# Kernel optimization log

Measured on AMD Instinct MI355X. Metric: run time of the kernel, lower is better.

Reference implementation:

```python
import jax, jax.numpy as jnp
import numpy as np

N_NODES = 250_000
N_EDGES = 1_250_000
N_CRY = 50_000
EMB = 200
FEA = 64
HID = 256
N_GRAPH = 3
ELEM_HEADS = 3
CRY_HEADS = 3


def _simple_net(x, w1, b1, w2, b2):
    # SimpleNetwork([d_in, 256, d_out]): Linear -> LeakyReLU -> Linear
    h = jax.nn.leaky_relu(x @ w1 + b1, negative_slope=0.01)
    return h @ w2 + b2


def setup_inputs() -> dict:
    key = jax.random.key(0)
    ks = jax.random.split(key, 32)
    s = 0.05
    inp = {
        # weights strictly positive (fractional stoichiometry weights)
        "elem_weights": jax.random.uniform(ks[0], (N_NODES, 1), jnp.float32) * 0.9 + 0.05,
        "elem_fea": jax.random.normal(ks[1], (N_NODES, EMB), jnp.float32),
        "self_fea_idx": jax.random.randint(ks[2], (N_EDGES,), 0, N_NODES),
        "nbr_fea_idx": jax.random.randint(ks[3], (N_EDGES,), 0, N_NODES),
        "cry_elem_idx": jnp.sort(jax.random.randint(ks[4], (N_NODES,), 0, N_CRY)),
        # embedding: Linear(EMB, FEA-1)
        "emb_w": jax.random.normal(ks[5], (EMB, FEA - 1), jnp.float32) * s,
        "emb_b": jnp.zeros((FEA - 1,), jnp.float32),
        # graph-layer attention heads (n_graph, elem_heads, ...)
        "g_gate_w1": jax.random.normal(ks[6], (N_GRAPH, ELEM_HEADS, 2 * FEA, HID), jnp.float32) * s,
        "g_gate_b1": jnp.zeros((N_GRAPH, ELEM_HEADS, HID), jnp.float32),
        "g_gate_w2": jax.random.normal(ks[7], (N_GRAPH, ELEM_HEADS, HID, 1), jnp.float32) * s,
        "g_gate_b2": jnp.zeros((N_GRAPH, ELEM_HEADS, 1), jnp.float32),
        "g_msg_w1": jax.random.normal(ks[8], (N_GRAPH, ELEM_HEADS, 2 * FEA, HID), jnp.float32) * s,
        "g_msg_b1": jnp.zeros((N_GRAPH, ELEM_HEADS, HID), jnp.float32),
        "g_msg_w2": jax.random.normal(ks[9], (N_GRAPH, ELEM_HEADS, HID, FEA), jnp.float32) * s,
        "g_msg_b2": jnp.zeros((N_GRAPH, ELEM_HEADS, FEA), jnp.float32),
        "g_pow": jax.random.normal(ks[10], (N_GRAPH, ELEM_HEADS), jnp.float32),
        # crystal pooling heads
        "c_gate_w1": jax.random.normal(ks[11], (CRY_HEADS, FEA, HID), jnp.float32) * s,
        "c_gate_b1": jnp.zeros((CRY_HEADS, HID), jnp.float32),
        "c_gate_w2": jax.random.normal(ks[12], (CRY_HEADS, HID, 1), jnp.float32) * s,
        "c_gate_b2": jnp.zeros((CRY_HEADS, 1), jnp.float32),
        "c_msg_w1": jax.random.normal(ks[13], (CRY_HEADS, FEA, HID), jnp.float32) * s,
        "c_msg_b1": jnp.zeros((CRY_HEADS, HID), jnp.float32),
        "c_msg_w2": jax.random.normal(ks[14], (CRY_HEADS, HID, FEA), jnp.float32) * s,
        "c_msg_b2": jnp.zeros((CRY_HEADS, FEA), jnp.float32),
        "c_pow": jax.random.normal(ks[15], (CRY_HEADS,), jnp.float32),
    }
    return inp


def _attn_pool(fea, weights, index, num_segments, gw1, gb1, gw2, gb2, mw1, mb1, mw2, mb2, p):
    # WeightedAttentionPooling: scatter-softmax with (weights ** pow) factor
    gate = _simple_net(fea, gw1, gb1, gw2, gb2)                       # (E, 1)
    gmax = jax.ops.segment_max(gate, index, num_segments=num_segments)
    gate = (weights ** p) * jnp.exp(gate - gmax[index])
    den = jax.ops.segment_sum(gate, index, num_segments=num_segments)
    gate = gate / (den[index] + 1e-10)
    msg = _simple_net(fea, mw1, mb1, mw2, mb2)                        # (E, FEA)
    return jax.ops.segment_sum(gate * msg, index, num_segments=num_segments)


def reference(elem_weights, elem_fea, self_fea_idx, nbr_fea_idx, cry_elem_idx,
              emb_w, emb_b,
              g_gate_w1, g_gate_b1, g_gate_w2, g_gate_b2,
              g_msg_w1, g_msg_b1, g_msg_w2, g_msg_b2, g_pow,
              c_gate_w1, c_gate_b1, c_gate_w2, c_gate_b2,
              c_msg_w1, c_msg_b1, c_msg_w2, c_msg_b2, c_pow):
    n = elem_fea.shape[0]
    x = elem_fea @ emb_w + emb_b                                      # (N, FEA-1)
    x = jnp.concatenate([x, elem_weights], axis=1)                    # (N, FEA)
    w_nbr = elem_weights[nbr_fea_idx]                                 # (M, 1)
    for l in range(g_pow.shape[0]):
        fea = jnp.concatenate([x[self_fea_idx], x[nbr_fea_idx]], axis=1)  # (M, 2*FEA)
        heads = []
        for h in range(g_pow.shape[1]):
            heads.append(_attn_pool(
                fea, w_nbr, self_fea_idx, n,
                g_gate_w1[l, h], g_gate_b1[l, h], g_gate_w2[l, h], g_gate_b2[l, h],
                g_msg_w1[l, h], g_msg_b1[l, h], g_msg_w2[l, h], g_msg_b2[l, h],
                g_pow[l, h]))
        x = jnp.mean(jnp.stack(heads), axis=0) + x                    # residual
    heads = []
    for h in range(c_pow.shape[0]):
        heads.append(_attn_pool(
            x, elem_weights, cry_elem_idx, N_CRY,
            c_gate_w1[h], c_gate_b1[h], c_gate_w2[h], c_gate_b2[h],
            c_msg_w1[h], c_msg_b1[h], c_msg_w2[h], c_msg_b2[h],
            c_pow[h]))
    return jnp.mean(jnp.stack(heads), axis=0)                         # (C, FEA)
```

## Files before the change

### kernel.cpp

```cpp
#include <hip/hip_runtime.h>
#include <math.h>

#define NN 250000
#define NE 1250000
#define NC 50000
#define EMBD 200
#define NCH 245
#define NBLK 22000
#define SSTR ((size_t)NBLK * 64)

typedef unsigned int u32;
typedef unsigned short u16;
typedef short s16x8 __attribute__((ext_vector_type(8)));
typedef float f32x4 __attribute__((ext_vector_type(4)));

__device__ __forceinline__ u16 f2bf(float f) {
    u32 u = __float_as_uint(f);
    return (u16)((u + 0x7FFFu + ((u >> 16) & 1u)) >> 16);
}
__device__ __forceinline__ float bf2f(u16 u) { return __uint_as_float(((u32)u) << 16); }
__device__ __forceinline__ u32 cvtpk(float lo, float hi) {
    u32 r;
    asm("v_cvt_pk_bf16_f32 %0, %1, %2" : "=v"(r) : "v"(lo), "v"(hi));
    return r;
}
__device__ __forceinline__ float lrelu(float v) { return v > 0.f ? v : 0.01f * v; }
__device__ __forceinline__ u32 encf(float f) {
    u32 u = __float_as_uint(f);
    return (u & 0x80000000u) ? ~u : (u | 0x80000000u);
}
__device__ __forceinline__ float decf(u32 k) {
    return __uint_as_float((k & 0x80000000u) ? (k ^ 0x80000000u) : ~k);
}

__global__ void k_pack(const float* __restrict__ src, u16* __restrict__ dst,
                       int K, int N, int nheads)
{
    const int t = blockIdx.x * 256 + threadIdx.x;
    const int F = (K / 32) * (N / 16);
    if (t >= nheads * F * 64) return;
    const int lane = t & 63;
    const int fh = t >> 6;
    const int f = fh % F, head = fh / F;
    const int ng = f % (N / 16), ks = f / (N / 16);
    const int q = lane >> 4, c = lane & 15;
    const float* s = src + (size_t)head * K * N;
    u16 o[8];
    #pragma unroll
    for (int i = 0; i < 8; ++i)
        o[i] = f2bf(s[(size_t)(32 * ks + 8 * q + i) * N + 16 * ng + c]);
    uint4 v;
    v.x = (u32)o[0] | ((u32)o[1] << 16);
    v.y = (u32)o[2] | ((u32)o[3] << 16);
    v.z = (u32)o[4] | ((u32)o[5] << 16);
    v.w = (u32)o[6] | ((u32)o[7] << 16);
    *(uint4*)(dst + (size_t)head * K * N + ((size_t)f * 64 + lane) * 8) = v;
// ... 119 lines not shown
            const int row = m * 16 + c;
            const int g = (ks * 4 + q) ^ (row & 7);
            s16x8 ah = *(const s16x8*)((const char*)Ahi + row * 512 + g * 16);
            s16x8 al = *(const s16x8*)((const char*)Alo + row * 512 + g * 16);
            acc[m] = __builtin_amdgcn_mfma_f32_16x16x32_bf16(ah, B[ks], acc[m], 0, 0, 0);
            acc[m] = __builtin_amdgcn_mfma_f32_16x16x32_bf16(al, B[ks], acc[m], 0, 0, 0);
        }
    }
    const int col = w * 16 + c;
    const float bv = (col < 63) ? emb_b[col] : 0.f;
    #pragma unroll
    for (int m = 0; m < 4; ++m)
        #pragma unroll
        for (int r = 0; r < 4; ++r) {
            const int node = n0 + m * 16 + q * 4 + r;
            if (node < NN) {
                const float val = (col < 63) ? acc[m][r] + bv : elem_w[node];
                x[(size_t)node * 64 + col] = val;
                xbf[(size_t)node * 64 + col] = f2bf(val);
            }
        }
}

__global__ void k_deg(const int* __restrict__ self_idx, int* __restrict__ deg) {
    int e = blockIdx.x * 256 + threadIdx.x;
    if (e < NE) atomicAdd(&deg[self_idx[e]], 1);
}

__global__ void k_nodepack(const int* __restrict__ deg, int* __restrict__ nstart,
                           int* __restrict__ ctotal)
{
    __shared__ int sdeg[1024];
    __shared__ int sst[1024];
    const int c0 = blockIdx.x << 10;
    const int cnt = min(1024, NN - c0);
    for (int i = threadIdx.x; i < cnt; i += 64) sdeg[i] = deg[c0 + i];
    __syncthreads();
    if (threadIdx.x == 0) {
        int cur = 0;
        for (int i = 0; i < cnt; ++i) {
            int d = sdeg[i];
            if (d > 0 && ((cur & 63) + d > 64)) cur = (cur + 63) & ~63;
            sst[i] = cur;
            cur += d;
        }
        ctotal[blockIdx.x] = (cur + 63) & ~63;
    }
    __syncthreads();
    for (int i = threadIdx.x; i < cnt; i += 64) nstart[c0 + i] = sst[i];
}

__global__ void k_chunkscan(const int* __restrict__ ctotal, int* __restrict__ cbase) {
    __shared__ int s[256];
    int t = threadIdx.x;
    int v = (t < NCH) ? ctotal[t] : 0;
    s[t] = v;
    __syncthreads();
    for (int off = 1; off < 256; off <<= 1) {
        int add = (t >= off) ? s[t - off] : 0;
        __syncthreads();
        s[t] += add;
        __syncthreads();
    }
    if (t < NCH) cbase[t] = s[t] - v;
}

__global__ void k_fill(const int* __restrict__ self_idx, const int* __restrict__ nbr_idx,
                       const float* __restrict__ elem_w,
                       const int* __restrict__ nstart, const int* __restrict__ cbase,
                       int* __restrict__ cursor, int2* __restrict__ gnode,
                       float* __restrict__ gwn)
{
    int e = blockIdx.x * 256 + threadIdx.x;
    if (e >= NE) return;
    int n = self_idx[e];
    int r = atomicAdd(&cursor[n], 1);
    int slot = cbase[n >> 10] + nstart[n] + r;
    int nb = nbr_idx[e];
    gnode[slot] = make_int2(n, nb);
    gwn[slot] = elem_w[nb];
}

__global__ __launch_bounds__(256, 4) void k_lgate(
    const u16* __restrict__ xbf, const int2* __restrict__ gnode,
    const float* __restrict__ gwn,
    const u16* __restrict__ gw1p, const float* __restrict__ gb1,
    const u16* __restrict__ gw2p, const float* __restrict__ gpw,
    float* __restrict__ sgf_out)
{
    __shared__ __align__(16) u16 sA[64 * 128];
    __shared__ __align__(16) u16 sH[64 * 128];
    __shared__ float sg[4][64];
    __shared__ float gfin[64], tval[64];
    __shared__ float swn[64];
    __shared__ int   snid[64];
    __shared__ short srs[64], sre[64];
    const int tid = threadIdx.x;
    const int base = blockIdx.x * 64;
    if (gnode[base].x < 0) return;

    if (tid < 64) {
        int2 nn = gnode[base + tid];
        snid[tid] = nn.x;
        swn[tid] = gwn[base + tid];
    }
    for (int i = tid; i < 64 * 16; i += 256) {
        const int row = i >> 4, g = i & 15;
        const int2 nn = gnode[base + row];
        const int node = (g < 8) ? nn.x : nn.y;
        uint4 v; v.x = 0; v.y = 0; v.z = 0; v.w = 0;
        if (node >= 0) v = *(const uint4*)(xbf + (size_t)node * 64 + (g & 7) * 8);
        *(uint4*)((char*)sA + row * 256 + ((g ^ (row & 7)) * 16)) = v;
    }
    __syncthreads();
    if (tid < 64) {
        int n = snid[tid];
        int rs = tid, re = tid + 1;
        if (n >= 0) {
            while (rs > 0 && snid[rs - 1] == n) --rs;
            while (re < 64 && snid[re] == n) ++re;
        }
        srs[tid] = (short)rs; sre[tid] = (short)re;
    }

    const int w = tid >> 6, lane = tid & 63, q = lane >> 4, c = lane & 15;

    #pragma unroll 1
    for (int h = 0; h < 3; ++h) {
        f32x4 acc2[4];
        #pragma unroll
        for (int m = 0; m < 4; ++m) acc2[m] = 0.f;
        const u16* wp = gw1p + (size_t)h * 128 * 256;
        #pragma unroll 1
        for (int half = 0; half < 2; ++half) {
            f32x4 acc[4][2];
            #pragma unroll
            for (int m = 0; m < 4; ++m) { acc[m][0] = 0.f; acc[m][1] = 0.f; }
            __builtin_amdgcn_s_setprio(1);
            #pragma unroll 2
            for (int ks = 0; ks < 4; ++ks) {
                s16x8 B1[2];
                #pragma unroll
                for (int n2 = 0; n2 < 2; ++n2)
                    B1[n2] = *(const s16x8*)(wp + ((size_t)(ks * 16 + w * 4 + half * 2 + n2) * 64 + lane) * 8);
                s16x8 a[4];
                #pragma unroll
                for (int m = 0; m < 4; ++m) {
                    const int row = m * 16 + c;
                    a[m] = *(const s16x8*)((const char*)sA + row * 256 + (((ks * 4 + q) ^ (row & 7)) * 16));
                }
                #pragma unroll
                for (int n2 = 0; n2 < 2; ++n2)
                    #pragma unroll
                    for (int m = 0; m < 4; ++m)
                        acc[m][n2] = __builtin_amdgcn_mfma_f32_16x16x32_bf16(a[m], B1[n2], acc[m][n2], 0, 0, 0);
            }
            __builtin_amdgcn_s_setprio(0);

            __syncthreads();
            const float b1a = gb1[h * 256 + w * 64 + (half * 2 + 0) * 16 + c];
            const float b1b = gb1[h * 256 + w * 64 + (half * 2 + 1) * 16 + c];
            #pragma unroll
            for (int m = 0; m < 4; ++m)
                #pragma unroll
                for (int r = 0; r < 4; ++r) {
                    const int row = m * 16 + q * 4 + r;
                    const u32 pk = cvtpk(lrelu(acc[m][0][r] + b1a), lrelu(acc[m][1][r] + b1b));
                    *(u32*)((char*)sH + row * 256 + (((w * 4 + (c >> 2)) ^ (row & 7)) * 16) + (c & 3) * 4) = pk;
                }
            s16x8 B2 = *(const s16x8*)(gw2p + ((size_t)(h * 8 + half * 4 + w) * 64 + lane) * 8);
            __syncthreads();

// ... 8 lines not shown
        }
        if (c == 0) {
            #pragma unroll
            for (int m = 0; m < 4; ++m)
                #pragma unroll
                for (int r = 0; r < 4; ++r)
                    sg[w][m * 16 + q * 4 + r] = acc2[m][r];
        }
        __syncthreads();
        if (tid < 64)
            gfin[tid] = (snid[tid] >= 0) ? sg[0][tid] + sg[1][tid] + sg[2][tid] + sg[3][tid] : -1e30f;
        __syncthreads();
        if (tid < 64) {
            const int rs = srs[tid], re = sre[tid];
            float m = -1e30f;
            for (int j = rs; j < re; ++j) m = fmaxf(m, gfin[j]);
            tval[tid] = (snid[tid] >= 0) ? powf(swn[tid], gpw[h]) * expf(gfin[tid] - m) : 0.f;
        }
        __syncthreads();
        if (tid < 64) {
            const int rs = srs[tid], re = sre[tid];
            float d = 1e-10f;
            for (int j = rs; j < re; ++j) d += tval[j];
            sgf_out[SSTR * h + base + tid] = tval[tid] / d;
        }
        __syncthreads();
    }
}

__global__ __launch_bounds__(256, 4) void k_lmsg(
    const u16* __restrict__ xbf, const int2* __restrict__ gnode,
    const u16* __restrict__ mw1p, const float* __restrict__ mb1,
    const u16* __restrict__ mw2p, const float* __restrict__ mb2,
    const float* __restrict__ sgf_in, float* __restrict__ pooled)
{
    __shared__ __align__(16) u16 sA[64 * 128];
    __shared__ __align__(16) u16 sH[64 * 128];
    __shared__ float sgfl[64][3];
    __shared__ int   snid[64];
    __shared__ short srs[64], sre[64];
    const int tid = threadIdx.x;
    const int base = blockIdx.x * 64;
    if (gnode[base].x < 0) return;

    if (tid < 64) snid[tid] = gnode[base + tid].x;
    if (tid < 192) {
        const int row = tid / 3, h = tid % 3;
        sgfl[row][h] = sgf_in[SSTR * h + base + row];
    }
    for (int i = tid; i < 64 * 16; i += 256) {
        const int row = i >> 4, g = i & 15;
        const int2 nn = gnode[base + row];
        const int node = (g < 8) ? nn.x : nn.y;
        uint4 v; v.x = 0; v.y = 0; v.z = 0; v.w = 0;
        if (node >= 0) v = *(const uint4*)(xbf + (size_t)node * 64 + (g & 7) * 8);
        *(uint4*)((char*)sA + row * 256 + ((g ^ (row & 7)) * 16)) = v;
    }
    __syncthreads();
    if (tid < 64) {
        int n = snid[tid];
        int rs = tid, re = tid + 1;
        if (n >= 0) {
            while (rs > 0 && snid[rs - 1] == n) --rs;
            while (re < 64 && snid[re] == n) ++re;
        }
        srs[tid] = (short)rs; sre[tid] = (short)re;
    }

    const int w = tid >> 6, lane = tid & 63, q = lane >> 4, c = lane & 15;
    float wacc[4][4];
    #pragma unroll
    for (int m = 0; m < 4; ++m)
        #pragma unroll
        for (int r = 0; r < 4; ++r) wacc[m][r] = 0.f;

    #pragma unroll 1
    for (int h = 0; h < 3; ++h) {
        const u16* wp = mw1p + (size_t)h * 128 * 256;
        #pragma unroll 1
        for (int half = 0; half < 2; ++half) {
            f32x4 acc[4][2];
            #pragma unroll
            for (int m = 0; m < 4; ++m) { acc[m][0] = 0.f; acc[m][1] = 0.f; }
            __builtin_amdgcn_s_setprio(1);
            #pragma unroll 2
            for (int ks = 0; ks < 4; ++ks) {
                s16x8 B1[2];
                #pragma unroll
                for (int n2 = 0; n2 < 2; ++n2)
                    B1[n2] = *(const s16x8*)(wp + ((size_t)(ks * 16 + w * 4 + half * 2 + n2) * 64 + lane) * 8);
                s16x8 a[4];
                #pragma unroll
                for (int m = 0; m < 4; ++m) {
                    const int row = m * 16 + c;
                    a[m] = *(const s16x8*)((const char*)sA + row * 256 + (((ks * 4 + q) ^ (row & 7)) * 16));
                }
                #pragma unroll
                for (int n2 = 0; n2 < 2; ++n2)
                    #pragma unroll
                    for (int m = 0; m < 4; ++m)
                        acc[m][n2] = __builtin_amdgcn_mfma_f32_16x16x32_bf16(a[m], B1[n2], acc[m][n2], 0, 0, 0);
            }
            __builtin_amdgcn_s_setprio(0);

            __syncthreads();
            const float b1a = mb1[h * 256 + w * 64 + (half * 2 + 0) * 16 + c];
            const float b1b = mb1[h * 256 + w * 64 + (half * 2 + 1) * 16 + c];
            #pragma unroll
            for (int m = 0; m < 4; ++m)
                #pragma unroll
                for (int r = 0; r < 4; ++r) {
                    const int row = m * 16 + q * 4 + r;
                    const u32 pk = cvtpk(lrelu(acc[m][0][r] + b1a), lrelu(acc[m][1][r] + b1b));
                    *(u32*)((char*)sH + row * 256 + (((w * 4 + (c >> 2)) ^ (row & 7)) * 16) + (c & 3) * 4) = pk;
                }
            s16x8 B2[4];
            #pragma unroll
            for (int k2 = 0; k2 < 4; ++k2)
// ... 21 lines not shown
                for (int r = 0; r < 4; ++r) {
                    const int row = m2 * 16 + q * 4 + r;
                    wacc[m2][r] += (acc2[m2][r] + b2v) * sgfl[row][h];
                }
        }
        __syncthreads();
    }

    float* waccL = (float*)sH;
    #pragma unroll
    for (int m = 0; m < 4; ++m)
        #pragma unroll
        for (int r = 0; r < 4; ++r)
            waccL[(m * 16 + q * 4 + r) * 64 + w * 16 + c] = wacc[m][r];
    __syncthreads();
    {
        const int col = tid & 63, grp = tid >> 6;
        for (int i = grp; i < 64; i += 4) {
            const int n = snid[i];
            if (n >= 0 && srs[i] == (short)i) {
                float s = 0.f;
                const int re = sre[i];
                for (int j = i; j < re; ++j) s += waccL[j * 64 + col];
                pooled[(size_t)n * 64 + col] = s * (1.f / 3.f);
            }
        }
    }
}

__global__ void k_mirror2(float* __restrict__ x, const float* __restrict__ pooled,
                          u16* __restrict__ xbf, int n4)
{
    int i = blockIdx.x * 256 + threadIdx.x;
    if (i >= n4) return;
    float4 xv = *(const float4*)(x + (size_t)i * 4);
    float4 pv = *(const float4*)(pooled + (size_t)i * 4);
    xv.x += pv.x; xv.y += pv.y; xv.z += pv.z; xv.w += pv.w;
    *(float4*)(x + (size_t)i * 4) = xv;
    uint2 o;
    o.x = cvtpk(xv.x, xv.y);
    o.y = cvtpk(xv.z, xv.w);
    *(uint2*)(xbf + (size_t)i * 4) = o;
}

template<int KD, bool GATHER>
__global__ __launch_bounds__(256, 4) void k_gate(
    const u16* __restrict__ xbf, const int* __restrict__ sidx, const int* __restrict__ nidx,
    const int* __restrict__ scat, const u16* __restrict__ w1p,
    const float* __restrict__ b1g, const float* __restrict__ w2g,
    float* __restrict__ gate_out, u32* __restrict__ gmax, int nrows, size_t gstride)
{
    constexpr int KS = KD / 32;
    constexpr int RB = KD * 2;
    constexpr int G  = KD / 8;
    __shared__ __align__(16) u16 sA[64 * KD];
    __shared__ float sg[4][64];
    const int tid = threadIdx.x;
    const int r0 = blockIdx.x * 64;
    const int rem = min(64, nrows - r0);

    for (int i = tid; i < 64 * G; i += 256) {
        const int row = i / G, g = i % G;
        const int rr = (row < rem) ? row : 0;
        uint4 v;
        if (GATHER) {
            const int node = (g < G / 2) ? sidx[r0 + rr] : nidx[r0 + rr];
            v = *(const uint4*)(xbf + (size_t)node * 64 + (g & (G / 2 - 1)) * 8);
        } else {
            v = *(const uint4*)(xbf + (size_t)(r0 + rr) * 64 + g * 8);
        }
        *(uint4*)((char*)sA + row * RB + ((g ^ (row & 7)) * 16)) = v;
    }
    __syncthreads();

    const int w = tid >> 6, lane = tid & 63, q = lane >> 4, c = lane & 15;

    #pragma unroll 1
    for (int h = 0; h < 3; ++h) {
        float part[4][4];
        #pragma unroll
        for (int m = 0; m < 4; ++m)
            #pragma unroll
            for (int r = 0; r < 4; ++r) part[m][r] = 0.f;
        const u16* wp = w1p + (size_t)h * KD * 256;
        #pragma unroll 1
        for (int half = 0; half < 2; ++half) {
            f32x4 acc[4][2];
            #pragma unroll
            for (int m = 0; m < 4; ++m) { acc[m][0] = 0.f; acc[m][1] = 0.f; }
            __builtin_amdgcn_s_setprio(1);
            #pragma unroll 2
            for (int ks = 0; ks < KS; ++ks) {
                s16x8 B1[2];
                #pragma unroll
                for (int n2 = 0; n2 < 2; ++n2)
                    B1[n2] = *(const s16x8*)(wp + ((size_t)(ks * 16 + w * 4 + half * 2 + n2) * 64 + lane) * 8);
                s16x8 a[4];
                #pragma unroll
                for (int m = 0; m < 4; ++m) {
                    const int row = m * 16 + c;
                    a[m] = *(const s16x8*)((const char*)sA + row * RB + (((ks * 4 + q) ^ (row & 7)) * 16));
                }
                #pragma unroll
                for (int n2 = 0; n2 < 2; ++n2)
                    #pragma unroll
                    for (int m = 0; m < 4; ++m)
                        acc[m][n2] = __builtin_amdgcn_mfma_f32_16x16x32_bf16(a[m], B1[n2], acc[m][n2], 0, 0, 0);
            }
            __builtin_amdgcn_s_setprio(0);
            #pragma unroll
            for (int n2 = 0; n2 < 2; ++n2) {
                const int col = w * 64 + (half * 2 + n2) * 16 + c;
                const float b1v = b1g[h * 256 + col];
                const float w2v = w2g[h * 256 + col];
                #pragma unroll
                for (int m = 0; m < 4; ++m)
                    #pragma unroll
                    for (int r = 0; r < 4; ++r)
                        part[m][r] += lrelu(acc[m][n2][r] + b1v) * w2v;
            }
        }
        #pragma unroll
        for (int off = 1; off < 16; off <<= 1)
            #pragma unroll
            for (int m = 0; m < 4; ++m)
                #pragma unroll
                for (int r = 0; r < 4; ++r)
                    part[m][r] += __shfl_xor(part[m][r], off, 64);
        if (c == 0) {
            #pragma unroll
            for (int m = 0; m < 4; ++m)
                #pragma unroll
                for (int r = 0; r < 4; ++r)
                    sg[w][m * 16 + q * 4 + r] = part[m][r];
        }
        __syncthreads();
        if (tid < rem) {
            const float gv = sg[0][tid] + sg[1][tid] + sg[2][tid] + sg[3][tid];
            gate_out[gstride * h + r0 + tid] = gv;
            atomicMax(&gmax[scat[r0 + tid] * 3 + h], encf(gv));
        }
        __syncthreads();
    }
}

template<int KD, bool GATHER>
__global__ __launch_bounds__(256, 4) void k_msg(
    const u16* __restrict__ xbf, const int* __restrict__ sidx, const int* __restrict__ nidx,
    const int* __restrict__ scat, const u16* __restrict__ w1p, const float* __restrict__ b1g,
    const u16* __restrict__ w2p, const float* __restrict__ b2g,
    const float* __restrict__ tbuf, const float* __restrict__ den,
    float* __restrict__ outp, int nrows, size_t gstride)
{
    constexpr int KS = KD / 32;
    constexpr int RB = KD * 2;
    constexpr int G  = KD / 8;
    __shared__ __align__(16) u16 sA[64 * KD];
    __shared__ __align__(16) u16 sH[64 * 128];
    __shared__ float sgf[64][3];
    __shared__ int ssi[64];
    const int tid = threadIdx.x;
    const int r0 = blockIdx.x * 64;
    const int rem = min(64, nrows - r0);

    for (int i = tid; i < 64 * G; i += 256) {
        const int row = i / G, g = i % G;
        const int rr = (row < rem) ? row : 0;
        uint4 v;
        if (GATHER) {
            const int node = (g < G / 2) ? sidx[r0 + rr] : nidx[r0 + rr];
            v = *(const uint4*)(xbf + (size_t)node * 64 + (g & (G / 2 - 1)) * 8);
        } else {
            v = *(const uint4*)(xbf + (size_t)(r0 + rr) * 64 + g * 8);
        }
        *(uint4*)((char*)sA + row * RB + ((g ^ (row & 7)) * 16)) = v;
    }
    if (tid < 64) ssi[tid] = (tid < rem) ? scat[r0 + tid] : 0;
    if (tid < 192) {
        const int row = tid / 3, h = tid % 3;
        if (row < rem) {
            const int s = scat[r0 + row] * 3 + h;
            sgf[row][h] = tbuf[gstride * h + r0 + row] / (den[s] + 1e-10f);
        } else {
            sgf[row][h] = 0.f;
        }
    }
    __syncthreads();

    const int w = tid >> 6, lane = tid & 63, q = lane >> 4, c = lane & 15;
    float wacc[4][4];
    #pragma unroll
    for (int m = 0; m < 4; ++m)
        #pragma unroll
        for (int r = 0; r < 4; ++r) wacc[m][r] = 0.f;

    #pragma unroll 1
    for (int h = 0; h < 3; ++h) {
        const u16* wp = w1p + (size_t)h * KD * 256;
        #pragma unroll 1
        for (int half = 0; half < 2; ++half) {
            f32x4 acc[4][2];
            #pragma unroll
            for (int m = 0; m < 4; ++m) { acc[m][0] = 0.f; acc[m][1] = 0.f; }
            __builtin_amdgcn_s_setprio(1);
            #pragma unroll 2
            for (int ks = 0; ks < KS; ++ks) {
                s16x8 B1[2];
                #pragma unroll
                for (int n2 = 0; n2 < 2; ++n2)
                    B1[n2] = *(const s16x8*)(wp + ((size_t)(ks * 16 + w * 4 + half * 2 + n2) * 64 + lane) * 8);
                s16x8 a[4];
                #pragma unroll
                for (int m = 0; m < 4; ++m) {
                    const int row = m * 16 + c;
                    a[m] = *(const s16x8*)((const char*)sA + row * RB + (((ks * 4 + q) ^ (row & 7)) * 16));
                }
                #pragma unroll
                for (int n2 = 0; n2 < 2; ++n2)
                    #pragma unroll
                    for (int m = 0; m < 4; ++m)
                        acc[m][n2] = __builtin_amdgcn_mfma_f32_16x16x32_bf16(a[m], B1[n2], acc[m][n2], 0, 0, 0);
            }
            __builtin_amdgcn_s_setprio(0);

            __syncthreads();
            const float b1a = b1g[h * 256 + w * 64 + (half * 2 + 0) * 16 + c];
            const float b1b = b1g[h * 256 + w * 64 + (half * 2 + 1) * 16 + c];
            #pragma unroll
            for (int m = 0; m < 4; ++m)
                #pragma unroll
                for (int r = 0; r < 4; ++r) {
                    const int row = m * 16 + q * 4 + r;
                    const u32 pk = cvtpk(lrelu(acc[m][0][r] + b1a), lrelu(acc[m][1][r] + b1b));
                    *(u32*)((char*)sH + row * 256 + (((w * 4 + (c >> 2)) ^ (row & 7)) * 16) + (c & 3) * 4) = pk;
                }
            s16x8 B2[4];
            #pragma unroll
            for (int k2 = 0; k2 < 4; ++k2)
                B2[k2] = *(const s16x8*)(w2p + (size_t)h * 256 * 64 + ((size_t)((half * 4 + k2) * 4 + w) * 64 + lane) * 8);
            __syncthreads();

            f32x4 acc2[4];
            #pragma unroll
            for (int m = 0; m < 4; ++m) acc2[m] = 0.f;
            __builtin_amdgcn_s_setprio(1);
            #pragma unroll
            for (int k2 = 0; k2 < 4; ++k2) {
                #pragma unroll
                for (int m2 = 0; m2 < 4; ++m2) {
                    const int row = m2 * 16 + c;
                    s16x8 a2 = *(const s16x8*)((const char*)sH + row * 256 + (((k2 * 4 + q) ^ (row & 7)) * 16));
                    acc2[m2] = __builtin_amdgcn_mfma_f32_16x16x32_bf16(a2, B2[k2], acc2[m2], 0, 0, 0);
                }
            }
            __builtin_amdgcn_s_setprio(0);
            const float b2v = half ? b2g[h * 64 + w * 16 + c] : 0.f;
            #pragma unroll
            for (int m2 = 0; m2 < 4; ++m2)
                #pragma unroll
                for (int r = 0; r < 4; ++r) {
                    const int row = m2 * 16 + q * 4 + r;
                    wacc[m2][r] += (acc2[m2][r] + b2v) * sgf[row][h];
                }
        }
    }
    #pragma unroll
    for (int m = 0; m < 4; ++m)
        #pragma unroll
        for (int r = 0; r < 4; ++r) {
            const int row = m * 16 + q * 4 + r;
            if (row < rem)
                atomicAdd(&outp[(size_t)ssi[row] * 64 + w * 16 + c], wacc[m][r] * (1.f / 3.f));
        }
}

__global__ void k_seg_exp(float* __restrict__ gate_t, const int* __restrict__ idx,
                          const int* __restrict__ wi, const float* __restrict__ elem_w,
                          const float* __restrict__ pw, const u32* __restrict__ gmax,
                          float* __restrict__ den, int n, size_t gstride)
{
    int e = blockIdx.x * blockDim.x + threadIdx.x;
    if (e >= n) return;
    int s = idx[e] * 3;
    float wgt = elem_w[wi ? wi[e] : e];
    #pragma unroll
    for (int h = 0; h < 3; ++h) {
        float gm = decf(gmax[s + h]);
        float t = powf(wgt, pw[h]) * expf(gate_t[gstride * h + e] - gm);
        gate_t[gstride * h + e] = t;
        atomicAdd(&den[s + h], t);
    }
}

extern "C" void kernel_launch(void* const* d_in, const int* in_sizes, int n_in,
                              void* d_out, int out_size, void* d_ws, size_t ws_size,
                              hipStream_t stream)
{
    const float* elem_w   = (const float*)d_in[0];
    const float* elem_fea = (const float*)d_in[1];
    const int*   self_idx = (const int*)d_in[2];
    const int*   nbr_idx  = (const int*)d_in[3];
    const int*   cry_idx  = (const int*)d_in[4];
    const float* emb_w    = (const float*)d_in[5];
    const float* emb_b    = (const float*)d_in[6];
    const float* gg_w1    = (const float*)d_in[7];
    const float* gg_b1    = (const float*)d_in[8];
    const float* gg_w2    = (const float*)d_in[9];
    const float* gm_w1    = (const float*)d_in[11];
    const float* gm_b1    = (const float*)d_in[12];
    const float* gm_w2    = (const float*)d_in[13];
    const float* gm_b2    = (const float*)d_in[14];
    const float* g_pow    = (const float*)d_in[15];
    const float* cg_w1    = (const float*)d_in[16];
    const float* cg_b1    = (const float*)d_in[17];
    const float* cg_w2    = (const float*)d_in[18];
    const float* cm_w1    = (const float*)d_in[20];
    const float* cm_b1    = (const float*)d_in[21];
    const float* cm_w2    = (const float*)d_in[22];
    const float* cm_b2    = (const float*)d_in[23];
    const float* c_pow    = (const float*)d_in[24];

    char* wsp = (char*)d_ws;
    size_t off = 0;
    auto alloc = [&](size_t b) { char* p = wsp + off; off += (b + 255) & ~(size_t)255; return p; };
    float* x      = (float*)alloc((size_t)NN * 64 * 4);
    float* pooled = (float*)alloc((size_t)NN * 64 * 4);
    u16*   xbf    = (u16*)  alloc((size_t)NN * 64 * 2);
    float* sgf    = (float*)alloc((size_t)3 * SSTR * 4);
    float* gate_t = (float*)alloc((size_t)NN * 3 * 4);
    float* cden   = (float*)alloc((size_t)NC * 3 * 4);
    u32*   cgmax  = (u32*)  alloc((size_t)NC * 3 * 4);
    int* deg    = (int*)alloc((size_t)NN * 4);
    int* nstart = (int*)alloc((size_t)NN * 4);
    int* cursor = (int*)alloc((size_t)NN * 4);
    int* ctotal = (int*)alloc((size_t)NCH * 4);
    int* cbase  = (int*)alloc((size_t)NCH * 4);
    int2* gnode = (int2*)alloc((size_t)NBLK * 64 * 8);
    float* gwn  = (float*)alloc((size_t)NBLK * 64 * 4);
    u16* wg1p = (u16*)alloc((size_t)9 * 128 * 256 * 2);
    u16* wm1p = (u16*)alloc((size_t)9 * 128 * 256 * 2);
    u16* wm2p = (u16*)alloc((size_t)9 * 256 * 64 * 2);
    u16* wg2p = (u16*)alloc((size_t)9 * 8 * 64 * 8 * 2);
    u16* cg1p = (u16*)alloc((size_t)3 * 64 * 256 * 2);
    u16* cm1p = (u16*)alloc((size_t)3 * 64 * 256 * 2);
    u16* cm2p = (u16*)alloc((size_t)3 * 256 * 64 * 2);
    u16* webp = (u16*)alloc((size_t)224 * 64 * 2);

    auto pack = [&](const float* s, u16* d, int K, int N, int H) {
        int tot = H * (K / 32) * (N / 16) * 64;
        k_pack<<<(tot + 255) / 256, 256, 0, stream>>>(s, d, K, N, H);
    };
    pack(gg_w1, wg1p, 128, 256, 9);
    pack(gm_w1, wm1p, 128, 256, 9);
    pack(cg_w1, cg1p, 64, 256, 3);
    pack(cm_w1, cm1p, 64, 256, 3);
    k_pack2<<<(9 * 32 * 64 + 255) / 256, 256, 0, stream>>>(gm_w2, wm2p, 9);
    k_pack2<<<(3 * 32 * 64 + 255) / 256, 256, 0, stream>>>(cm_w2, cm2p, 3);
    k_packg<<<(9 * 8 * 64 + 255) / 256, 256, 0, stream>>>(gg_w2, wg2p, 9);
    k_packe<<<7, 256, 0, stream>>>(emb_w, webp);

    hipMemsetAsync(deg, 0, (size_t)NN * 4, stream);
    hipMemsetAsync(cursor, 0, (size_t)NN * 4, stream);
    hipMemsetAsync(gnode, 0xFF, (size_t)NBLK * 64 * 8, stream);
    k_deg<<<(NE + 255) / 256, 256, 0, stream>>>(self_idx, deg);
    k_nodepack<<<NCH, 64, 0, stream>>>(deg, nstart, ctotal);
    k_chunkscan<<<1, 256, 0, stream>>>(ctotal, cbase);
    k_fill<<<(NE + 255) / 256, 256, 0, stream>>>(self_idx, nbr_idx, elem_w,
                                                 nstart, cbase, cursor, gnode, gwn);

    k_embed_mm<<<(NN + 63) / 64, 256, 0, stream>>>(elem_fea, elem_w, webp, emb_b, x, xbf);

    for (int l = 0; l < 3; ++l) {
        hipMemsetAsync(pooled, 0, (size_t)NN * 64 * 4, stream);
        k_lgate<<<NBLK, 256, 0, stream>>>(
            xbf, gnode, gwn,
            wg1p + (size_t)l * 3 * 128 * 256, gg_b1 + l * 768,
            wg2p + (size_t)l * 3 * 8 * 64 * 8, g_pow + l * 3, sgf);
        k_lmsg<<<NBLK, 256, 0, stream>>>(
            xbf, gnode,
            wm1p + (size_t)l * 3 * 128 * 256, gm_b1 + l * 768,
            wm2p + (size_t)l * 3 * 256 * 64, gm_b2 + l * 192, sgf, pooled);
        k_mirror2<<<(NN * 64 / 4 + 255) / 256, 256, 0, stream>>>(x, pooled, xbf, NN * 64 / 4);
    }

    hipMemsetAsync(cgmax, 0, (size_t)NC * 3 * 4, stream);
    hipMemsetAsync(cden, 0, (size_t)NC * 3 * 4, stream);
    hipMemsetAsync(d_out, 0, (size_t)NC * 64 * 4, stream);
    const int GN = (NN + 63) / 64;
    k_gate<64, false><<<GN, 256, 0, stream>>>(
        xbf, nullptr, nullptr, cry_idx, cg1p, cg_b1, cg_w2, gate_t, cgmax, NN, (size_t)NN);
    k_seg_exp<<<(NN + 255) / 256, 256, 0, stream>>>(
        gate_t, cry_idx, nullptr, elem_w, c_pow, cgmax, cden, NN, (size_t)NN);
    k_msg<64, false><<<GN, 256, 0, stream>>>(
        xbf, nullptr, nullptr, cry_idx, cm1p, cm_b1, cm2p, cm_b2,
        gate_t, cden, (float*)d_out, NN, (size_t)NN);
}
```

Before: 3.988 ms.

## Reuse segment-packed gate/msg kernels for crystal pooling and fuse residual add

Builds a segment-packed layout (blocks of 64 rows aligned to crystal boundaries) for the crystal pooling stage, so the templated in-block softmax gate and message kernels replace the old atomicMax/seg_exp/atomicAdd three-kernel path. The layer message kernel now adds directly into x, which removes the pooled buffer, its memset and the residual add in the mirror kernel. This costs extra setup kernels and some padding rows, and the crystal path now needs every crystal segment to fit within 64 rows.

```diff
diff --git a/kernel.cpp b/kernel.cpp
--- a/kernel.cpp
+++ b/kernel.cpp
@@ -5,9 +5,12 @@
 #define NE 1250000
 #define NC 50000
 #define EMBD 200
-#define NCH 245
+#define NCH_E 245
+#define NCH_C 49
 #define NBLK 22000
-#define SSTR ((size_t)NBLK * 64)
+#define NCBLK 6000
+#define SSTR  ((size_t)NBLK * 64)
+#define SSTRC ((size_t)NCBLK * 64)
 
 typedef unsigned int u32;
 typedef unsigned short u16;
@@ -25,13 +28,6 @@
     return r;
 }
 __device__ __forceinline__ float lrelu(float v) { return v > 0.f ? v : 0.01f * v; }
-__device__ __forceinline__ u32 encf(float f) {
-    u32 u = __float_as_uint(f);
-    return (u & 0x80000000u) ? ~u : (u | 0x80000000u);
-}
-__device__ __forceinline__ float decf(u32 k) {
-    return __uint_as_float((k & 0x80000000u) ? (k ^ 0x80000000u) : ~k);
-}
 
 __global__ void k_pack(const float* __restrict__ src, u16* __restrict__ dst,
                        int K, int N, int nheads)
@@ -197,18 +193,18 @@
         }
 }
 
-__global__ void k_deg(const int* __restrict__ self_idx, int* __restrict__ deg) {
+__global__ void k_deg(const int* __restrict__ idx, int* __restrict__ deg, int n) {
     int e = blockIdx.x * 256 + threadIdx.x;
-    if (e < NE) atomicAdd(&deg[self_idx[e]], 1);
+    if (e < n) atomicAdd(&deg[idx[e]], 1);
 }
 
 __global__ void k_nodepack(const int* __restrict__ deg, int* __restrict__ nstart,
-                           int* __restrict__ ctotal)
+                           int* __restrict__ ctotal, int total_n)
 {
     __shared__ int sdeg[1024];
     __shared__ int sst[1024];
     const int c0 = blockIdx.x << 10;
-    const int cnt = min(1024, NN - c0);
+    const int cnt = min(1024, total_n - c0);
     for (int i = threadIdx.x; i < cnt; i += 64) sdeg[i] = deg[c0 + i];
     __syncthreads();
     if (threadIdx.x == 0) {
@@ -225,10 +221,10 @@
     for (int i = threadIdx.x; i < cnt; i += 64) nstart[c0 + i] = sst[i];
 }
 
-__global__ void k_chunkscan(const int* __restrict__ ctotal, int* __restrict__ cbase) {
+__global__ void k_chunkscan(const int* __restrict__ ctotal, int* __restrict__ cbase, int nch) {
     __shared__ int s[256];
     int t = threadIdx.x;
-    int v = (t < NCH) ? ctotal[t] : 0;
+    int v = (t < nch) ? ctotal[t] : 0;
     s[t] = v;
     __syncthreads();
     for (int off = 1; off < 256; off <<= 1) {
@@ -237,7 +233,7 @@
         s[t] += add;
         __syncthreads();
     }
-    if (t < NCH) cbase[t] = s[t] - v;
+    if (t < nch) cbase[t] = s[t] - v;
 }
 
 __global__ void k_fill(const int* __restrict__ self_idx, const int* __restrict__ nbr_idx,
@@ -256,14 +252,32 @@
     gwn[slot] = elem_w[nb];
 }
 
+__global__ void k_cfill(const int* __restrict__ cry_idx, const float* __restrict__ elem_w,
+                        const int* __restrict__ nstart, const int* __restrict__ cbase,
+                        int* __restrict__ cursor, int2* __restrict__ gnode,
+                        float* __restrict__ gwn)
+{
+    int n = blockIdx.x * 256 + threadIdx.x;
+    if (n >= NN) return;
+    int cg = cry_idx[n];
+    int r = atomicAdd(&cursor[cg], 1);
+    int slot = cbase[cg >> 10] + nstart[cg] + r;
+    gnode[slot] = make_int2(cg, n);
+    gwn[slot] = elem_w[n];
+}
+
+template<int KD>
 __global__ __launch_bounds__(256, 4) void k_lgate(
     const u16* __restrict__ xbf, const int2* __restrict__ gnode,
     const float* __restrict__ gwn,
     const u16* __restrict__ gw1p, const float* __restrict__ gb1,
     const u16* __restrict__ gw2p, const float* __restrict__ gpw,
-    float* __restrict__ sgf_out)
-{
-    __shared__ __align__(16) u16 sA[64 * 128];
+    float* __restrict__ sgf_out, size_t sstr)
+{
+    constexpr int KS = KD / 32;
+    constexpr int G  = KD / 8;
+    constexpr int RB = KD * 2;
+    __shared__ __align__(16) u16 sA[64 * KD];
     __shared__ __align__(16) u16 sH[64 * 128];
     __shared__ float sg[4][64];
     __shared__ float gfin[64], tval[64];
@@ -279,13 +293,13 @@
         snid[tid] = nn.x;
         swn[tid] = gwn[base + tid];
     }
-    for (int i = tid; i < 64 * 16; i += 256) {
-        const int row = i >> 4, g = i & 15;
+    for (int i = tid; i < 64 * G; i += 256) {
+        const int row = i / G, g = i % G;
         const int2 nn = gnode[base + row];
-        const int node = (g < 8) ? nn.x : nn.y;
+        const int node = (KD == 128) ? ((g < 8) ? nn.x : nn.y) : nn.y;
         uint4 v; v.x = 0; v.y = 0; v.z = 0; v.w = 0;
         if (node >= 0) v = *(const uint4*)(xbf + (size_t)node * 64 + (g & 7) * 8);
-        *(uint4*)((char*)sA + row * 256 + ((g ^ (row & 7)) * 16)) = v;
+        *(uint4*)((char*)sA + row * RB + ((g ^ (row & 7)) * 16)) = v;
     }
     __syncthreads();
     if (tid < 64) {
@@ -305,7 +319,7 @@
         f32x4 acc2[4];
         #pragma unroll
         for (int m = 0; m < 4; ++m) acc2[m] = 0.f;
-        const u16* wp = gw1p + (size_t)h * 128 * 256;
+        const u16* wp = gw1p + (size_t)h * KD * 256;
         #pragma unroll 1
         for (int half = 0; half < 2; ++half) {
             f32x4 acc[4][2];
@@ -313,7 +327,7 @@
             for (int m = 0; m < 4; ++m) { acc[m][0] = 0.f; acc[m][1] = 0.f; }
             __builtin_amdgcn_s_setprio(1);
             #pragma unroll 2
-            for (int ks = 0; ks < 4; ++ks) {
+            for (int ks = 0; ks < KS; ++ks) {
                 s16x8 B1[2];
                 #pragma unroll
                 for (int n2 = 0; n2 < 2; ++n2)
@@ -322,7 +336,7 @@
                 #pragma unroll
                 for (int m = 0; m < 4; ++m) {
                     const int row = m * 16 + c;
-                    a[m] = *(const s16x8*)((const char*)sA + row * 256 + (((ks * 4 + q) ^ (row & 7)) * 16));
+                    a[m] = *(const s16x8*)((const char*)sA + row * RB + (((ks * 4 + q) ^ (row & 7)) * 16));
                 }
                 #pragma unroll
                 for (int n2 = 0; n2 < 2; ++n2)
@@ -377,19 +391,23 @@
             const int rs = srs[tid], re = sre[tid];
             float d = 1e-10f;
             for (int j = rs; j < re; ++j) d += tval[j];
-            sgf_out[SSTR * h + base + tid] = tval[tid] / d;
+            sgf_out[sstr * h + base + tid] = tval[tid] / d;
         }
         __syncthreads();
     }
 }
 
+template<int KD, bool RESID>
 __global__ __launch_bounds__(256, 4) void k_lmsg(
     const u16* __restrict__ xbf, const int2* __restrict__ gnode,
     const u16* __restrict__ mw1p, const float* __restrict__ mb1,
     const u16* __restrict__ mw2p, const float* __restrict__ mb2,
-    const float* __restrict__ sgf_in, float* __restrict__ pooled)
-{
-    __shared__ __align__(16) u16 sA[64 * 128];
+    const float* __restrict__ sgf_in, float* __restrict__ outp, size_t sstr)
+{
+    constexpr int KS = KD / 32;
+    constexpr int G  = KD / 8;
+    constexpr int RB = KD * 2;
+    __shared__ __align__(16) u16 sA[64 * KD];
     __shared__ __align__(16) u16 sH[64 * 128];
     __shared__ float sgfl[64][3];
     __shared__ int   snid[64];
@@ -401,15 +419,15 @@
     if (tid < 64) snid[tid] = gnode[base + tid].x;
     if (tid < 192) {
         const int row = tid / 3, h = tid % 3;
-        sgfl[row][h] = sgf_in[SSTR * h + base + row];
-    }
-    for (int i = tid; i < 64 * 16; i += 256) {
-        const int row = i >> 4, g = i & 15;
+        sgfl[row][h] = sgf_in[sstr * h + base + row];
+    }
+    for (int i = tid; i < 64 * G; i += 256) {
+        const int row = i / G, g = i % G;
         const int2 nn = gnode[base + row];
-        const int node = (g < 8) ? nn.x : nn.y;
+        const int node = (KD == 128) ? ((g < 8) ? nn.x : nn.y) : nn.y;
         uint4 v; v.x = 0; v.y = 0; v.z = 0; v.w = 0;
         if (node >= 0) v = *(const uint4*)(xbf + (size_t)node * 64 + (g & 7) * 8);
-        *(uint4*)((char*)sA + row * 256 + ((g ^ (row & 7)) * 16)) = v;
+        *(uint4*)((char*)sA + row * RB + ((g ^ (row & 7)) * 16)) = v;
     }
     __syncthreads();
     if (tid < 64) {
@@ -431,7 +449,7 @@
 
     #pragma unroll 1
     for (int h = 0; h < 3; ++h) {
-        const u16* wp = mw1p + (size_t)h * 128 * 256;
+        const u16* wp = mw1p + (size_t)h * KD * 256;
         #pragma unroll 1
         for (int half = 0; half < 2; ++half) {
             f32x4 acc[4][2];
@@ -439,7 +457,7 @@
             for (int m = 0; m < 4; ++m) { acc[m][0] = 0.f; acc[m][1] = 0.f; }
             __builtin_amdgcn_s_setprio(1);
             #pragma unroll 2
-            for (int ks = 0; ks < 4; ++ks) {
+            for (int ks = 0; ks < KS; ++ks) {
                 s16x8 B1[2];
                 #pragma unroll
                 for (int n2 = 0; n2 < 2; ++n2)
@@ -448,7 +466,7 @@
                 #pragma unroll
                 for (int m = 0; m < 4; ++m) {
                     const int row = m * 16 + c;
-                    a[m] = *(const s16x8*)((const char*)sA + row * 256 + (((ks * 4 + q) ^ (row & 7)) * 16));
+                    a[m] = *(const s16x8*)((const char*)sA + row * RB + (((ks * 4 + q) ^ (row & 7)) * 16));
                 }
                 #pragma unroll
                 for (int n2 = 0; n2 < 2; ++n2)
@@ -516,274 +534,22 @@
                 float s = 0.f;
                 const int re = sre[i];
                 for (int j = i; j < re; ++j) s += waccL[j * 64 + col];
-                pooled[(size_t)n * 64 + col] = s * (1.f / 3.f);
+                if (RESID) outp[(size_t)n * 64 + col] += s * (1.f / 3.f);
+                else       outp[(size_t)n * 64 + col]  = s * (1.f / 3.f);
             }
         }
     }
 }
 
-__global__ void k_mirror2(float* __restrict__ x, const float* __restrict__ pooled,
-                          u16* __restrict__ xbf, int n4)
+__global__ void k_mirror(const float* __restrict__ x, u16* __restrict__ xbf, int n4)
 {
     int i = blockIdx.x * 256 + threadIdx.x;
     if (i >= n4) return;
     float4 xv = *(const float4*)(x + (size_t)i * 4);
-    float4 pv = *(const float4*)(pooled + (size_t)i * 4);
-    xv.x += pv.x; xv.y += pv.y; xv.z += pv.z; xv.w += pv.w;
-    *(float4*)(x + (size_t)i * 4) = xv;
     uint2 o;
     o.x = cvtpk(xv.x, xv.y);
     o.y = cvtpk(xv.z, xv.w);
     *(uint2*)(xbf + (size_t)i * 4) = o;
-}
-
-template<int KD, bool GATHER>
-__global__ __launch_bounds__(256, 4) void k_gate(
-    const u16* __restrict__ xbf, const int* __restrict__ sidx, const int* __restrict__ nidx,
-    const int* __restrict__ scat, const u16* __restrict__ w1p,
-    const float* __restrict__ b1g, const float* __restrict__ w2g,
-    float* __restrict__ gate_out, u32* __restrict__ gmax, int nrows, size_t gstride)
-{
-    constexpr int KS = KD / 32;
-    constexpr int RB = KD * 2;
-    constexpr int G  = KD / 8;
-    __shared__ __align__(16) u16 sA[64 * KD];
-    __shared__ float sg[4][64];
-    const int tid = threadIdx.x;
-    const int r0 = blockIdx.x * 64;
-    const int rem = min(64, nrows - r0);
-
-    for (int i = tid; i < 64 * G; i += 256) {
-        const int row = i / G, g = i % G;
-        const int rr = (row < rem) ? row : 0;
-        uint4 v;
-        if (GATHER) {
-            const int node = (g < G / 2) ? sidx[r0 + rr] : nidx[r0 + rr];
-            v = *(const uint4*)(xbf + (size_t)node * 64 + (g & (G / 2 - 1)) * 8);
-        } else {
-            v = *(const uint4*)(xbf + (size_t)(r0 + rr) * 64 + g * 8);
-        }
-        *(uint4*)((char*)sA + row * RB + ((g ^ (row & 7)) * 16)) = v;
-    }
-    __syncthreads();
-
-    const int w = tid >> 6, lane = tid & 63, q = lane >> 4, c = lane & 15;
-
-    #pragma unroll 1
-    for (int h = 0; h < 3; ++h) {
-        float part[4][4];
-        #pragma unroll
-        for (int m = 0; m < 4; ++m)
-            #pragma unroll
-            for (int r = 0; r < 4; ++r) part[m][r] = 0.f;
-        const u16* wp = w1p + (size_t)h * KD * 256;
-        #pragma unroll 1
-        for (int half = 0; half < 2; ++half) {
-            f32x4 acc[4][2];
-            #pragma unroll
-            for (int m = 0; m < 4; ++m) { acc[m][0] = 0.f; acc[m][1] = 0.f; }
-            __builtin_amdgcn_s_setprio(1);
-            #pragma unroll 2
-            for (int ks = 0; ks < KS; ++ks) {
-                s16x8 B1[2];
-                #pragma unroll
-                for (int n2 = 0; n2 < 2; ++n2)
-                    B1[n2] = *(const s16x8*)(wp + ((size_t)(ks * 16 + w * 4 + half * 2 + n2) * 64 + lane) * 8);
-                s16x8 a[4];
-                #pragma unroll
-                for (int m = 0; m < 4; ++m) {
-                    const int row = m * 16 + c;
-                    a[m] = *(const s16x8*)((const char*)sA + row * RB + (((ks * 4 + q) ^ (row & 7)) * 16));
-                }
-                #pragma unroll
-                for (int n2 = 0; n2 < 2; ++n2)
-                    #pragma unroll
-                    for (int m = 0; m < 4; ++m)
-                        acc[m][n2] = __builtin_amdgcn_mfma_f32_16x16x32_bf16(a[m], B1[n2], acc[m][n2], 0, 0, 0);
-            }
-            __builtin_amdgcn_s_setprio(0);
-            #pragma unroll
-            for (int n2 = 0; n2 < 2; ++n2) {
-                const int col = w * 64 + (half * 2 + n2) * 16 + c;
-                const float b1v = b1g[h * 256 + col];
-                const float w2v = w2g[h * 256 + col];
-                #pragma unroll
-                for (int m = 0; m < 4; ++m)
-                    #pragma unroll
-                    for (int r = 0; r < 4; ++r)
-                        part[m][r] += lrelu(acc[m][n2][r] + b1v) * w2v;
-            }
-        }
-        #pragma unroll
-        for (int off = 1; off < 16; off <<= 1)
-            #pragma unroll
-            for (int m = 0; m < 4; ++m)
-                #pragma unroll
-                for (int r = 0; r < 4; ++r)
-                    part[m][r] += __shfl_xor(part[m][r], off, 64);
-        if (c == 0) {
-            #pragma unroll
-            for (int m = 0; m < 4; ++m)
-                #pragma unroll
-                for (int r = 0; r < 4; ++r)
-                    sg[w][m * 16 + q * 4 + r] = part[m][r];
-        }
-        __syncthreads();
-        if (tid < rem) {
-            const float gv = sg[0][tid] + sg[1][tid] + sg[2][tid] + sg[3][tid];
-            gate_out[gstride * h + r0 + tid] = gv;
-            atomicMax(&gmax[scat[r0 + tid] * 3 + h], encf(gv));
-        }
-        __syncthreads();
-    }
-}
-
-template<int KD, bool GATHER>
-__global__ __launch_bounds__(256, 4) void k_msg(
-    const u16* __restrict__ xbf, const int* __restrict__ sidx, const int* __restrict__ nidx,
-    const int* __restrict__ scat, const u16* __restrict__ w1p, const float* __restrict__ b1g,
-    const u16* __restrict__ w2p, const float* __restrict__ b2g,
-    const float* __restrict__ tbuf, const float* __restrict__ den,
-    float* __restrict__ outp, int nrows, size_t gstride)
-{
-    constexpr int KS = KD / 32;
-    constexpr int RB = KD * 2;
-    constexpr int G  = KD / 8;
-    __shared__ __align__(16) u16 sA[64 * KD];
-    __shared__ __align__(16) u16 sH[64 * 128];
-    __shared__ float sgf[64][3];
-    __shared__ int ssi[64];
-    const int tid = threadIdx.x;
-    const int r0 = blockIdx.x * 64;
-    const int rem = min(64, nrows - r0);
-
-    for (int i = tid; i < 64 * G; i += 256) {
-        const int row = i / G, g = i % G;
-        const int rr = (row < rem) ? row : 0;
-        uint4 v;
-        if (GATHER) {
-            const int node = (g < G / 2) ? sidx[r0 + rr] : nidx[r0 + rr];
-            v = *(const uint4*)(xbf + (size_t)node * 64 + (g & (G / 2 - 1)) * 8);
-        } else {
-            v = *(const uint4*)(xbf + (size_t)(r0 + rr) * 64 + g * 8);
-        }
-        *(uint4*)((char*)sA + row * RB + ((g ^ (row & 7)) * 16)) = v;
-    }
-    if (tid < 64) ssi[tid] = (tid < rem) ? scat[r0 + tid] : 0;
-    if (tid < 192) {
-        const int row = tid / 3, h = tid % 3;
-        if (row < rem) {
-            const int s = scat[r0 + row] * 3 + h;
-            sgf[row][h] = tbuf[gstride * h + r0 + row] / (den[s] + 1e-10f);
-        } else {
-            sgf[row][h] = 0.f;
-        }
-    }
-    __syncthreads();
-
-    const int w = tid >> 6, lane = tid & 63, q = lane >> 4, c = lane & 15;
-    float wacc[4][4];
-    #pragma unroll
-    for (int m = 0; m < 4; ++m)
-        #pragma unroll
-        for (int r = 0; r < 4; ++r) wacc[m][r] = 0.f;
-
-    #pragma unroll 1
-    for (int h = 0; h < 3; ++h) {
-        const u16* wp = w1p + (size_t)h * KD * 256;
-        #pragma unroll 1
-        for (int half = 0; half < 2; ++half) {
-            f32x4 acc[4][2];
-            #pragma unroll
-            for (int m = 0; m < 4; ++m) { acc[m][0] = 0.f; acc[m][1] = 0.f; }
-            __builtin_amdgcn_s_setprio(1);
-            #pragma unroll 2
-            for (int ks = 0; ks < KS; ++ks) {
-                s16x8 B1[2];
-                #pragma unroll
-                for (int n2 = 0; n2 < 2; ++n2)
-                    B1[n2] = *(const s16x8*)(wp + ((size_t)(ks * 16 + w * 4 + half * 2 + n2) * 64 + lane) * 8);
-                s16x8 a[4];
-                #pragma unroll
-                for (int m = 0; m < 4; ++m) {
-                    const int row = m * 16 + c;
-                    a[m] = *(const s16x8*)((const char*)sA + row * RB + (((ks * 4 + q) ^ (row & 7)) * 16));
-                }
-                #pragma unroll
-                for (int n2 = 0; n2 < 2; ++n2)
-                    #pragma unroll
-                    for (int m = 0; m < 4; ++m)
-                        acc[m][n2] = __builtin_amdgcn_mfma_f32_16x16x32_bf16(a[m], B1[n2], acc[m][n2], 0, 0, 0);
-            }
-            __builtin_amdgcn_s_setprio(0);
-
-            __syncthreads();
-            const float b1a = b1g[h * 256 + w * 64 + (half * 2 + 0) * 16 + c];
-            const float b1b = b1g[h * 256 + w * 64 + (half * 2 + 1) * 16 + c];
-            #pragma unroll
-            for (int m = 0; m < 4; ++m)
-                #pragma unroll
-                for (int r = 0; r < 4; ++r) {
-                    const int row = m * 16 + q * 4 + r;
-                    const u32 pk = cvtpk(lrelu(acc[m][0][r] + b1a), lrelu(acc[m][1][r] + b1b));
-                    *(u32*)((char*)sH + row * 256 + (((w * 4 + (c >> 2)) ^ (row & 7)) * 16) + (c & 3) * 4) = pk;
-                }
-            s16x8 B2[4];
-            #pragma unroll
-            for (int k2 = 0; k2 < 4; ++k2)
-                B2[k2] = *(const s16x8*)(w2p + (size_t)h * 256 * 64 + ((size_t)((half * 4 + k2) * 4 + w) * 64 + lane) * 8);
-            __syncthreads();
-
-            f32x4 acc2[4];
-            #pragma unroll
-            for (int m = 0; m < 4; ++m) acc2[m] = 0.f;
-            __builtin_amdgcn_s_setprio(1);
-            #pragma unroll
-            for (int k2 = 0; k2 < 4; ++k2) {
-                #pragma unroll
-                for (int m2 = 0; m2 < 4; ++m2) {
-                    const int row = m2 * 16 + c;
-                    s16x8 a2 = *(const s16x8*)((const char*)sH + row * 256 + (((k2 * 4 + q) ^ (row & 7)) * 16));
-                    acc2[m2] = __builtin_amdgcn_mfma_f32_16x16x32_bf16(a2, B2[k2], acc2[m2], 0, 0, 0);
-                }
-            }
-            __builtin_amdgcn_s_setprio(0);
-            const float b2v = half ? b2g[h * 64 + w * 16 + c] : 0.f;
-            #pragma unroll
-            for (int m2 = 0; m2 < 4; ++m2)
-                #pragma unroll
-                for (int r = 0; r < 4; ++r) {
-                    const int row = m2 * 16 + q * 4 + r;
-                    wacc[m2][r] += (acc2[m2][r] + b2v) * sgf[row][h];
-                }
-        }
-    }
-    #pragma unroll
-    for (int m = 0; m < 4; ++m)
-        #pragma unroll
-        for (int r = 0; r < 4; ++r) {
-            const int row = m * 16 + q * 4 + r;
-            if (row < rem)
-                atomicAdd(&outp[(size_t)ssi[row] * 64 + w * 16 + c], wacc[m][r] * (1.f / 3.f));
-        }
-}
-
-__global__ void k_seg_exp(float* __restrict__ gate_t, const int* __restrict__ idx,
-                          const int* __restrict__ wi, const float* __restrict__ elem_w,
-                          const float* __restrict__ pw, const u32* __restrict__ gmax,
-                          float* __restrict__ den, int n, size_t gstride)
-{
-    int e = blockIdx.x * blockDim.x + threadIdx.x;
-    if (e >= n) return;
-    int s = idx[e] * 3;
-    float wgt = elem_w[wi ? wi[e] : e];
-    #pragma unroll
-    for (int h = 0; h < 3; ++h) {
-        float gm = decf(gmax[s + h]);
-        float t = powf(wgt, pw[h]) * expf(gate_t[gstride * h + e] - gm);
-        gate_t[gstride * h + e] = t;
-        atomicAdd(&den[s + h], t);
-    }
 }
 
 extern "C" void kernel_launch(void* const* d_in, const int* in_sizes, int n_in,
@@ -818,19 +584,23 @@
     size_t off = 0;
     auto alloc = [&](size_t b) { char* p = wsp + off; off += (b + 255) & ~(size_t)255; return p; };
     float* x      = (float*)alloc((size_t)NN * 64 * 4);
-    float* pooled = (float*)alloc((size_t)NN * 64 * 4);
     u16*   xbf    = (u16*)  alloc((size_t)NN * 64 * 2);
     float* sgf    = (float*)alloc((size_t)3 * SSTR * 4);
-    float* gate_t = (float*)alloc((size_t)NN * 3 * 4);
-    float* cden   = (float*)alloc((size_t)NC * 3 * 4);
-    u32*   cgmax  = (u32*)  alloc((size_t)NC * 3 * 4);
+    float* csgf   = (float*)alloc((size_t)3 * SSTRC * 4);
     int* deg    = (int*)alloc((size_t)NN * 4);
     int* nstart = (int*)alloc((size_t)NN * 4);
     int* cursor = (int*)alloc((size_t)NN * 4);
-    int* ctotal = (int*)alloc((size_t)NCH * 4);
-    int* cbase  = (int*)alloc((size_t)NCH * 4);
+    int* ctotal = (int*)alloc((size_t)NCH_E * 4);
+    int* cbase  = (int*)alloc((size_t)NCH_E * 4);
     int2* gnode = (int2*)alloc((size_t)NBLK * 64 * 8);
     float* gwn  = (float*)alloc((size_t)NBLK * 64 * 4);
+    int* cdeg    = (int*)alloc((size_t)NC * 4);
+    int* cnstart = (int*)alloc((size_t)NC * 4);
+    int* ccursor = (int*)alloc((size_t)NC * 4);
+    int* cctotal = (int*)alloc((size_t)NCH_C * 4);
+    int* ccbase  = (int*)alloc((size_t)NCH_C * 4);
+    int2* cgnode = (int2*)alloc((size_t)NCBLK * 64 * 8);
+    float* cgwn  = (float*)alloc((size_t)NCBLK * 64 * 4);
     u16* wg1p = (u16*)alloc((size_t)9 * 128 * 256 * 2);
     u16* wm1p = (u16*)alloc((size_t)9 * 128 * 256 * 2);
     u16* wm2p = (u16*)alloc((size_t)9 * 256 * 64 * 2);
@@ -838,6 +608,7 @@
     u16* cg1p = (u16*)alloc((size_t)3 * 64 * 256 * 2);
     u16* cm1p = (u16*)alloc((size_t)3 * 64 * 256 * 2);
     u16* cm2p = (u16*)alloc((size_t)3 * 256 * 64 * 2);
+    u16* cg2p = (u16*)alloc((size_t)3 * 8 * 64 * 8 * 2);
     u16* webp = (u16*)alloc((size_t)224 * 64 * 2);
 
     auto pack = [&](const float* s, u16* d, int K, int N, int H) {
@@ -851,41 +622,43 @@
     k_pack2<<<(9 * 32 * 64 + 255) / 256, 256, 0, stream>>>(gm_w2, wm2p, 9);
     k_pack2<<<(3 * 32 * 64 + 255) / 256, 256, 0, stream>>>(cm_w2, cm2p, 3);
     k_packg<<<(9 * 8 * 64 + 255) / 256, 256, 0, stream>>>(gg_w2, wg2p, 9);
+    k_packg<<<(3 * 8 * 64 + 255) / 256, 256, 0, stream>>>(cg_w2, cg2p, 3);
     k_packe<<<7, 256, 0, stream>>>(emb_w, webp);
 
     hipMemsetAsync(deg, 0, (size_t)NN * 4, stream);
     hipMemsetAsync(cursor, 0, (size_t)NN * 4, stream);
     hipMemsetAsync(gnode, 0xFF, (size_t)NBLK * 64 * 8, stream);
-    k_deg<<<(NE + 255) / 256, 256, 0, stream>>>(self_idx, deg);
-    k_nodepack<<<NCH, 64, 0, stream>>>(deg, nstart, ctotal);
-    k_chunkscan<<<1, 256, 0, stream>>>(ctotal, cbase);
+    k_deg<<<(NE + 255) / 256, 256, 0, stream>>>(self_idx, deg, NE);
+    k_nodepack<<<NCH_E, 64, 0, stream>>>(deg, nstart, ctotal, NN);
+    k_chunkscan<<<1, 256, 0, stream>>>(ctotal, cbase, NCH_E);
     k_fill<<<(NE + 255) / 256, 256, 0, stream>>>(self_idx, nbr_idx, elem_w,
                                                  nstart, cbase, cursor, gnode, gwn);
+    hipMemsetAsync(cdeg, 0, (size_t)NC * 4, stream);
+    hipMemsetAsync(ccursor, 0, (size_t)NC * 4, stream);
+    hipMemsetAsync(cgnode, 0xFF, (size_t)NCBLK * 64 * 8, stream);
+    k_deg<<<(NN + 255) / 256, 256, 0, stream>>>(cry_idx, cdeg, NN);
+    k_nodepack<<<NCH_C, 64, 0, stream>>>(cdeg, cnstart, cctotal, NC);
+    k_chunkscan<<<1, 256, 0, stream>>>(cctotal, ccbase, NCH_C);
+    k_cfill<<<(NN + 255) / 256, 256, 0, stream>>>(cry_idx, elem_w,
+                                                  cnstart, ccbase, ccursor, cgnode, cgwn);
 
     k_embed_mm<<<(NN + 63) / 64, 256, 0, stream>>>(elem_fea, elem_w, webp, emb_b, x, xbf);
 
     for (int l = 0; l < 3; ++l) {
-        hipMemsetAsync(pooled, 0, (size_t)NN * 64 * 4, stream);
-        k_lgate<<<NBLK, 256, 0, stream>>>(
+        k_lgate<128><<<NBLK, 256, 0, stream>>>(
             xbf, gnode, gwn,
             wg1p + (size_t)l * 3 * 128 * 256, gg_b1 + l * 768,
-            wg2p + (size_t)l * 3 * 8 * 64 * 8, g_pow + l * 3, sgf);
-        k_lmsg<<<NBLK, 256, 0, stream>>>(
+            wg2p + (size_t)l * 3 * 8 * 64 * 8, g_pow + l * 3, sgf, SSTR);
+        k_lmsg<128, true><<<NBLK, 256, 0, stream>>>(
             xbf, gnode,
             wm1p + (size_t)l * 3 * 128 * 256, gm_b1 + l * 768,
-            wm2p + (size_t)l * 3 * 256 * 64, gm_b2 + l * 192, sgf, pooled);
-        k_mirror2<<<(NN * 64 / 4 + 255) / 256, 256, 0, stream>>>(x, pooled, xbf, NN * 64 / 4);
-    }
-
-    hipMemsetAsync(cgmax, 0, (size_t)NC * 3 * 4, stream);
-    hipMemsetAsync(cden, 0, (size_t)NC * 3 * 4, stream);
+            wm2p + (size_t)l * 3 * 256 * 64, gm_b2 + l * 192, sgf, x, SSTR);
+        k_mirror<<<(NN * 64 / 4 + 255) / 256, 256, 0, stream>>>(x, xbf, NN * 64 / 4);
+    }
+
     hipMemsetAsync(d_out, 0, (size_t)NC * 64 * 4, stream);
-    const int GN = (NN + 63) / 64;
-    k_gate<64, false><<<GN, 256, 0, stream>>>(
-        xbf, nullptr, nullptr, cry_idx, cg1p, cg_b1, cg_w2, gate_t, cgmax, NN, (size_t)NN);
-    k_seg_exp<<<(NN + 255) / 256, 256, 0, stream>>>(
-        gate_t, cry_idx, nullptr, elem_w, c_pow, cgmax, cden, NN, (size_t)NN);
-    k_msg<64, false><<<GN, 256, 0, stream>>>(
-        xbf, nullptr, nullptr, cry_idx, cm1p, cm_b1, cm2p, cm_b2,
-        gate_t, cden, (float*)d_out, NN, (size_t)NN);
-}
+    k_lgate<64><<<NCBLK, 256, 0, stream>>>(
+        xbf, cgnode, cgwn, cg1p, cg_b1, cg2p, c_pow, csgf, SSTRC);
+    k_lmsg<64, false><<<NCBLK, 256, 0, stream>>>(
+        xbf, cgnode, cm1p, cm_b1, cm2p, cm_b2, csgf, (float*)d_out, SSTRC);
+}
```

Result: no change. 4.033 ms (+1.1%).
